# Optimization experiments

Measured on AMD Instinct MI355X. Metric: run time of the kernel, lower is better.

The kernel has to match this reference:

```python
import jax, jax.numpy as jnp
import numpy as np

WIN = 9
EPS = 1e-05


def _box_sum(x, win):
    """Depthwise win x win box-filter sum with SAME padding, via two separable 1D convs."""
    C = x.shape[1]
    pad = win // 2
    dn = ('NCHW', 'OIHW', 'NCHW')
    kh = jnp.ones((C, 1, win, 1), dtype=x.dtype)
    kw = jnp.ones((C, 1, 1, win), dtype=x.dtype)
    x = jax.lax.conv_general_dilated(x, kh, (1, 1), [(pad, pad), (0, 0)],
                                     dimension_numbers=dn, feature_group_count=C)
    x = jax.lax.conv_general_dilated(x, kw, (1, 1), [(0, 0), (pad, pad)],
                                     dimension_numbers=dn, feature_group_count=C)
    return x


def setup_inputs() -> dict:
    key = jax.random.key(0)
    k1, k2 = jax.random.split(key)
    B, C, H, W = 32, 4, 512, 512
    y_pred = jax.random.uniform(k1, (B, C, H, W), dtype=jnp.float32)
    y_true = jax.random.uniform(k2, (B, C, H, W), dtype=jnp.float32)
    return {"y_pred": y_pred, "y_true": y_true}


def reference(y_pred, y_true):
    C = y_true.shape[1]
    n = float(WIN * WIN)
    # Stack the 5 moment maps along channels -> one fused box-filter pass.
    stacked = jnp.concatenate(
        [y_true, y_pred, y_true * y_true, y_pred * y_pred, y_true * y_pred], axis=1)
    sums = _box_sum(stacked, WIN)
    sum_I, sum_J, sum_I2, sum_J2, sum_IJ = jnp.split(sums, 5, axis=1)
    mu_I = sum_I / n
    mu_J = sum_J / n
    var_I = sum_I2 / n - mu_I * mu_I
    var_J = sum_J2 / n - mu_J * mu_J
    cov_IJ = sum_IJ / n - mu_I * mu_J
    cc = cov_IJ * cov_IJ / (jnp.maximum(var_I, 0.0) * jnp.maximum(var_J, 0.0) + EPS)
    return -jnp.mean(cc)
```

## Files before the change

### kernel.cpp

```cpp
#include <hip/hip_runtime.h>


#define PAD 4
#define EPS 1e-5f

constexpr int B = 32, C = 4, H = 512, W = 512;
constexpr int ROWS = 32;
constexpr int TPB = 128;
constexpr int CPT = 4;
constexpr int SLOTS = 528;
constexpr int NCHUNK = H / ROWS;
constexpr int NBLK = B * C * NCHUNK;
constexpr float INV_N = 1.0f / 81.0f;

template <bool ADD>
__device__ __forceinline__ void accrow(const float* __restrict__ I,
                                       const float* __restrict__ J,
                                       int r, int x0,
                                       float sI[CPT], float sJ[CPT],
                                       float sI2[CPT], float sJ2[CPT],
                                       float sIJ[CPT]) {
    const float4 vi = *(const float4*)(I + (size_t)r * W + x0);
    const float4 vj = *(const float4*)(J + (size_t)r * W + x0);
    float fi[CPT] = {vi.x, vi.y, vi.z, vi.w};
    float fj[CPT] = {vj.x, vj.y, vj.z, vj.w};
#pragma unroll
    for (int k = 0; k < CPT; ++k) {
        float a = fi[k], b = fj[k];
        if (ADD) {
            sI[k] += a; sJ[k] += b;
            sI2[k] += a * a; sJ2[k] += b * b; sIJ[k] += a * b;
        } else {
            sI[k] -= a; sJ[k] -= b;
            sI2[k] -= a * a; sJ2[k] -= b * b; sIJ[k] -= a * b;
        }
    }
}

__global__ __launch_bounds__(TPB) void ncc_partial(
        const float* __restrict__ y_pred, const float* __restrict__ y_true,
        float* __restrict__ partial) {
    __shared__ float vs[5][SLOTS];
    __shared__ float wsum[TPB / 64];

    const int bid = blockIdx.x;
    const int chunk = bid % NCHUNK;
    const int plane = bid / NCHUNK;
    const size_t base = (size_t)plane * H * W;
    const float* I = y_true + base;
    const float* J = y_pred + base;

    const int t = threadIdx.x;
    const int x0 = t * CPT;

    if (t < 2 * PAD) {
        int s = (t < PAD) ? t : (512 + t);
#pragma unroll
        for (int ch = 0; ch < 5; ++ch) vs[ch][s] = 0.0f;
    }

    const int y0 = chunk * ROWS;

    float sI[CPT] = {0.f, 0.f, 0.f, 0.f}, sJ[CPT] = {0.f, 0.f, 0.f, 0.f};
    float sI2[CPT] = {0.f, 0.f, 0.f, 0.f}, sJ2[CPT] = {0.f, 0.f, 0.f, 0.f};
    float sIJ[CPT] = {0.f, 0.f, 0.f, 0.f};

    for (int r = y0 - PAD; r < y0 + PAD; ++r) {
        if (r >= 0 && r < H)
            accrow<true>(I, J, r, x0, sI, sJ, sI2, sJ2, sIJ);
    }

    float acc = 0.0f;

    for (int yo = 0; yo < ROWS; ++yo) {
        const int y = y0 + yo;
        const int rin = y + PAD;
        if (rin < H) accrow<true>(I, J, rin, x0, sI, sJ, sI2, sJ2, sIJ);

        __syncthreads();
        *(float4*)&vs[0][x0 + PAD] = make_float4(sI[0], sI[1], sI[2], sI[3]);
        *(float4*)&vs[1][x0 + PAD] = make_float4(sJ[0], sJ[1], sJ[2], sJ[3]);
        *(float4*)&vs[2][x0 + PAD] = make_float4(sI2[0], sI2[1], sI2[2], sI2[3]);
        *(float4*)&vs[3][x0 + PAD] = make_float4(sJ2[0], sJ2[1], sJ2[2], sJ2[3]);
        *(float4*)&vs[4][x0 + PAD] = make_float4(sIJ[0], sIJ[1], sIJ[2], sIJ[3]);
        __syncthreads();

        float h[5][CPT];
#pragma unroll
        for (int ch = 0; ch < 5; ++ch) {
            const float* row = vs[ch];
            const float4 a = *(const float4*)(row + x0);
            const float4 b = *(const float4*)(row + x0 + 4);
            const float4 c = *(const float4*)(row + x0 + 8);
            float s = a.x + a.y + a.z + a.w + b.x + b.y + b.z + b.w + c.x;
            h[ch][0] = s;
            s += c.y - a.x; h[ch][1] = s;
            s += c.z - a.y; h[ch][2] = s;
            s += c.w - a.z; h[ch][3] = s;
        }

#pragma unroll
        for (int k = 0; k < CPT; ++k) {
            const float mI = h[0][k] * INV_N;
            const float mJ = h[1][k] * INV_N;
            const float vI = h[2][k] * INV_N - mI * mI;
            const float vJ = h[3][k] * INV_N - mJ * mJ;
            const float cv = h[4][k] * INV_N - mI * mJ;
            const float den = fmaxf(vI, 0.0f) * fmaxf(vJ, 0.0f) + EPS;
            acc += cv * cv / den;
        }

        const int rout = y - PAD;
        if (rout >= 0) accrow<false>(I, J, rout, x0, sI, sJ, sI2, sJ2, sIJ);
    }

#pragma unroll
    for (int off = 32; off > 0; off >>= 1)
        acc += __shfl_down(acc, off, 64);
    __syncthreads();
    if ((t & 63) == 0) wsum[t >> 6] = acc;
    __syncthreads();
    if (t == 0) partial[bid] = wsum[0] + wsum[1];
}

__global__ __launch_bounds__(256) void ncc_final(
        const float* __restrict__ partial, float* __restrict__ out) {
    const int t = threadIdx.x;
    float s = 0.0f;
    for (int i = t; i < NBLK; i += 256) s += partial[i];
    __shared__ float ws[4];
#pragma unroll
    for (int off = 32; off > 0; off >>= 1)
        s += __shfl_down(s, off, 64);
    if ((t & 63) == 0) ws[t >> 6] = s;
    __syncthreads();
    if (t == 0) {
        const float tot = ws[0] + ws[1] + ws[2] + ws[3];
        out[0] = -tot / (float)((long long)B * C * H * W);
    }
}

extern "C" void kernel_launch(void* const* d_in, const int* in_sizes, int n_in,
                              void* d_out, int out_size, void* d_ws, size_t ws_size,
                              hipStream_t stream) {
    const float* y_pred = (const float*)d_in[0];
    const float* y_true = (const float*)d_in[1];
    float* out = (float*)d_out;
    float* partial = (float*)d_ws;

    ncc_partial<<<NBLK, TPB, 0, stream>>>(y_pred, y_true, partial);
    ncc_final<<<1, 256, 0, stream>>>(partial, out);
}
```

Baseline: 96.79 us.

## Double-buffer shared row sums, widen blocks to 256 threads with 2 columns each

```diff
diff --git a/kernel.cpp b/kernel.cpp
--- a/kernel.cpp
+++ b/kernel.cpp
@@ -6,33 +6,31 @@
 
 constexpr int B = 32, C = 4, H = 512, W = 512;
 constexpr int ROWS = 32;
-constexpr int TPB = 128;
-constexpr int CPT = 4;
-constexpr int SLOTS = 528;
+constexpr int TPB = 256;
+constexpr int CPT = 2;
+constexpr int SLOTS = 520;
 constexpr int NCHUNK = H / ROWS;
 constexpr int NBLK = B * C * NCHUNK;
+constexpr int NPART = NBLK * 4;
 constexpr float INV_N = 1.0f / 81.0f;
 
 template <bool ADD>
 __device__ __forceinline__ void accrow(const float* __restrict__ I,
                                        const float* __restrict__ J,
-                                       int r, int x0,
-                                       float sI[CPT], float sJ[CPT],
-                                       float sI2[CPT], float sJ2[CPT],
-                                       float sIJ[CPT]) {
-    const float4 vi = *(const float4*)(I + (size_t)r * W + x0);
-    const float4 vj = *(const float4*)(J + (size_t)r * W + x0);
-    float fi[CPT] = {vi.x, vi.y, vi.z, vi.w};
-    float fj[CPT] = {vj.x, vj.y, vj.z, vj.w};
+                                       int r, int x0, float s[5][CPT]) {
+    const float2 vi = *(const float2*)(I + (size_t)r * W + x0);
+    const float2 vj = *(const float2*)(J + (size_t)r * W + x0);
+    float fi[CPT] = {vi.x, vi.y};
+    float fj[CPT] = {vj.x, vj.y};
 #pragma unroll
     for (int k = 0; k < CPT; ++k) {
         float a = fi[k], b = fj[k];
         if (ADD) {
-            sI[k] += a; sJ[k] += b;
-            sI2[k] += a * a; sJ2[k] += b * b; sIJ[k] += a * b;
+            s[0][k] += a; s[1][k] += b;
+            s[2][k] += a * a; s[3][k] += b * b; s[4][k] += a * b;
         } else {
-            sI[k] -= a; sJ[k] -= b;
-            sI2[k] -= a * a; sJ2[k] -= b * b; sIJ[k] -= a * b;
+            s[0][k] -= a; s[1][k] -= b;
+            s[2][k] -= a * a; s[3][k] -= b * b; s[4][k] -= a * b;
         }
     }
 }
@@ -40,8 +38,7 @@
 __global__ __launch_bounds__(TPB) void ncc_partial(
         const float* __restrict__ y_pred, const float* __restrict__ y_true,
         float* __restrict__ partial) {
-    __shared__ float vs[5][SLOTS];
-    __shared__ float wsum[TPB / 64];
+    __shared__ float vs[2][5][SLOTS];
 
     const int bid = blockIdx.x;
     const int chunk = bid % NCHUNK;
@@ -54,20 +51,19 @@
     const int x0 = t * CPT;
 
     if (t < 2 * PAD) {
-        int s = (t < PAD) ? t : (512 + t);
+        const int sl = (t < PAD) ? t : (512 + t);
 #pragma unroll
-        for (int ch = 0; ch < 5; ++ch) vs[ch][s] = 0.0f;
+        for (int b = 0; b < 2; ++b)
+#pragma unroll
+            for (int ch = 0; ch < 5; ++ch) vs[b][ch][sl] = 0.0f;
     }
 
     const int y0 = chunk * ROWS;
 
-    float sI[CPT] = {0.f, 0.f, 0.f, 0.f}, sJ[CPT] = {0.f, 0.f, 0.f, 0.f};
-    float sI2[CPT] = {0.f, 0.f, 0.f, 0.f}, sJ2[CPT] = {0.f, 0.f, 0.f, 0.f};
-    float sIJ[CPT] = {0.f, 0.f, 0.f, 0.f};
+    float s[5][CPT] = {{0.f, 0.f}, {0.f, 0.f}, {0.f, 0.f}, {0.f, 0.f}, {0.f, 0.f}};
 
     for (int r = y0 - PAD; r < y0 + PAD; ++r) {
-        if (r >= 0 && r < H)
-            accrow<true>(I, J, r, x0, sI, sJ, sI2, sJ2, sIJ);
+        if (r >= 0 && r < H) accrow<true>(I, J, r, x0, s);
     }
 
     float acc = 0.0f;
@@ -75,28 +71,27 @@
     for (int yo = 0; yo < ROWS; ++yo) {
         const int y = y0 + yo;
         const int rin = y + PAD;
-        if (rin < H) accrow<true>(I, J, rin, x0, sI, sJ, sI2, sJ2, sIJ);
+        if (rin < H) accrow<true>(I, J, rin, x0, s);
 
-        __syncthreads();
-        *(float4*)&vs[0][x0 + PAD] = make_float4(sI[0], sI[1], sI[2], sI[3]);
-        *(float4*)&vs[1][x0 + PAD] = make_float4(sJ[0], sJ[1], sJ[2], sJ[3]);
-        *(float4*)&vs[2][x0 + PAD] = make_float4(sI2[0], sI2[1], sI2[2], sI2[3]);
-        *(float4*)&vs[3][x0 + PAD] = make_float4(sJ2[0], sJ2[1], sJ2[2], sJ2[3]);
-        *(float4*)&vs[4][x0 + PAD] = make_float4(sIJ[0], sIJ[1], sIJ[2], sIJ[3]);
+        float (* const vb)[SLOTS] = vs[yo & 1];
+#pragma unroll
+        for (int ch = 0; ch < 5; ++ch)
+            *(float2*)&vb[ch][x0 + PAD] = make_float2(s[ch][0], s[ch][1]);
         __syncthreads();
 
         float h[5][CPT];
 #pragma unroll
         for (int ch = 0; ch < 5; ++ch) {
-            const float* row = vs[ch];
-            const float4 a = *(const float4*)(row + x0);
-            const float4 b = *(const float4*)(row + x0 + 4);
-            const float4 c = *(const float4*)(row + x0 + 8);
-            float s = a.x + a.y + a.z + a.w + b.x + b.y + b.z + b.w + c.x;
-            h[ch][0] = s;
-            s += c.y - a.x; h[ch][1] = s;
-            s += c.z - a.y; h[ch][2] = s;
-            s += c.w - a.z; h[ch][3] = s;
+            const float* row = vb[ch];
+            const float2 r0 = *(const float2*)(row + x0);
+            const float2 r1 = *(const float2*)(row + x0 + 2);
+            const float2 r2 = *(const float2*)(row + x0 + 4);
+            const float2 r3 = *(const float2*)(row + x0 + 6);
+            const float2 r4 = *(const float2*)(row + x0 + 8);
+            const float s0 = r0.x + r0.y + r1.x + r1.y + r2.x + r2.y +
+                             r3.x + r3.y + r4.x;
+            h[ch][0] = s0;
+            h[ch][1] = s0 + r4.y - r0.x;
         }
 
 #pragma unroll
@@ -111,28 +106,25 @@
         }
 
         const int rout = y - PAD;
-        if (rout >= 0) accrow<false>(I, J, rout, x0, sI, sJ, sI2, sJ2, sIJ);
+        if (rout >= 0) accrow<false>(I, J, rout, x0, s);
     }
 
 #pragma unroll
     for (int off = 32; off > 0; off >>= 1)
         acc += __shfl_down(acc, off, 64);
-    __syncthreads();
-    if ((t & 63) == 0) wsum[t >> 6] = acc;
-    __syncthreads();
-    if (t == 0) partial[bid] = wsum[0] + wsum[1];
+    if ((t & 63) == 0) partial[bid * 4 + (t >> 6)] = acc;
 }
 
 __global__ __launch_bounds__(256) void ncc_final(
         const float* __restrict__ partial, float* __restrict__ out) {
     const int t = threadIdx.x;
-    float s = 0.0f;
-    for (int i = t; i < NBLK; i += 256) s += partial[i];
+    float sum = 0.0f;
+    for (int i = t; i < NPART; i += 256) sum += partial[i];
     __shared__ float ws[4];
 #pragma unroll
     for (int off = 32; off > 0; off >>= 1)
-        s += __shfl_down(s, off, 64);
-    if ((t & 63) == 0) ws[t >> 6] = s;
+        sum += __shfl_down(sum, off, 64);
+    if ((t & 63) == 0) ws[t >> 6] = sum;
     __syncthreads();
     if (t == 0) {
         const float tot = ws[0] + ws[1] + ws[2] + ws[3];
```

Measured after the change: 115.6 us. 19.5% more time.
